# Optimization experiments

Measured on AMD Instinct MI355X. Metric: run time of the kernel, lower is better.

Reference implementation:

```python
import jax, jax.numpy as jnp
import numpy as np

H, D, HID = 16, 128, 2048
B, S = 2, 2048
NUM_BLOCKS, BLOCK_SIZE = 32, 128


def _rope(x, cos, sin):
    # x: [T, H, D]; cos/sin: [T, D/2] (neox / rotate-half style)
    half = x.shape[-1] // 2
    x1, x2 = x[..., :half], x[..., half:]
    c = cos[:, None, :]
    s = sin[:, None, :]
    return jnp.concatenate([x1 * c - x2 * s, x2 * c + x1 * s], axis=-1)


def setup_inputs() -> dict:
    key = jax.random.key(0)
    ks = jax.random.split(key, 6)
    T = B * S
    hidden_states = jax.random.normal(ks[0], (T, HID), jnp.float32)
    wqkv = jax.random.normal(ks[1], (HID, 3 * HID), jnp.float32) * 0.02
    bqkv = jax.random.normal(ks[2], (3 * HID,), jnp.float32) * 0.02
    wo = jax.random.normal(ks[3], (HID, HID), jnp.float32) * 0.02
    # rotary tables, base 10000, dim = head_size
    inv_freq = 1.0 / (10000.0 ** (jnp.arange(0, D, 2, dtype=jnp.float32) / D))  # [D/2]
    pos = jnp.tile(jnp.arange(S, dtype=jnp.float32), B)  # positions per token [T]
    ang = pos[:, None] * inv_freq[None, :]  # [T, D/2]
    cos, sin = jnp.cos(ang), jnp.sin(ang)
    k_cache = jnp.zeros((NUM_BLOCKS, BLOCK_SIZE, H, D), jnp.float32)
    v_cache = jnp.zeros((NUM_BLOCKS, BLOCK_SIZE, H, D), jnp.float32)
    cu_seqlen_prefill = jnp.array([0, S, 2 * S], jnp.int32)
    slots = jnp.arange(T, dtype=jnp.int32)
    return {"hidden_states": hidden_states, "cos": cos, "sin": sin,
            "wqkv": wqkv, "bqkv": bqkv, "wo": wo,
            "k_cache": k_cache, "v_cache": v_cache,
            "cu_seqlen_prefill": cu_seqlen_prefill, "slots": slots, "max_s": S}


def reference(hidden_states, cos, sin, wqkv, bqkv, wo, k_cache, v_cache,
              cu_seqlen_prefill, slots, max_s):
    T = hidden_states.shape[0]
    # fused QKV projection (c_attn)
    qkv = hidden_states @ wqkv + bqkv  # [T, 3*H*D]
    q, k, v = jnp.split(qkv, [H * D, 2 * H * D], axis=1)
    q = q.reshape(T, H, D)
    k = k.reshape(T, H, D)
    v = v.reshape(T, H, D)
    # rotary embedding on q and k (in-place in torch; functional here)
    q = _rope(q, cos, sin)
    k = _rope(k, cos, sin)
    # reshape_and_cache: scatter post-rope k and v into paged KV cache by slot
    kc = k_cache.reshape(-1, H, D).at[slots].set(k).reshape(k_cache.shape)
    vc = v_cache.reshape(-1, H, D).at[slots].set(v).reshape(v_cache.shape)
    # prefill flash attention: varlen causal; equal-length sequences here
    b, s = T // max_s, max_s
    qb = q.reshape(b, s, H, D)
    kb = k.reshape(b, s, H, D)
    vb = v.reshape(b, s, H, D)
    scale = D ** -0.5
    scores = jnp.einsum('bqhd,bkhd->bhqk', qb, kb) * scale  # [B,H,S,S]
    causal = jnp.tril(jnp.ones((s, s), bool))
    scores = jnp.where(causal[None, None], scores, jnp.finfo(scores.dtype).min)
    probs = jax.nn.softmax(scores, axis=-1)
    attn = jnp.einsum('bhqk,bkhd->bqhd', probs, vb).reshape(T, H * D)
    out = attn @ wo  # c_proj, no bias
    return out, kc, vc
```

## Files before the change

### kernel.cpp

```cpp
#include <hip/hip_runtime.h>

using f32x4  = __attribute__((ext_vector_type(4))) float;
using frag16 = __attribute__((ext_vector_type(8))) short;
using s16x4  = __attribute__((ext_vector_type(4))) short;
using s16x8  = __attribute__((ext_vector_type(8))) short;
using u32x4  = __attribute__((ext_vector_type(4))) unsigned;

#define DI __device__ __forceinline__

constexpr int HID  = 2048;
constexpr int NH   = 16;
constexpr int HD   = 128;
constexpr int TT   = 4096;
constexpr int SEQ  = 2048;
constexpr int NQKV = 3 * HID;
constexpr float SCL = 0.08838834764831845f * 1.4426950408889634f;

DI short f2bf(float f) {
  unsigned u = __builtin_bit_cast(unsigned, f);
  unsigned r = (u + 0x7fffu + ((u >> 16) & 1u)) >> 16;
  return (short)r;
}
DI float bf2f(short s) {
  unsigned u = ((unsigned)(unsigned short)s) << 16;
  return __builtin_bit_cast(float, u);
}
DI unsigned cvtpk(float lo, float hi) {
  unsigned r;
  asm("v_cvt_pk_bf16_f32 %0, %1, %2" : "=v"(r) : "v"(lo), "v"(hi));
  return r;
}

struct alignas(8) S4h { short a, b, c, d; };

__global__ void prep(const float* __restrict__ hidden, short* __restrict__ Abf,
                     const float* __restrict__ wqkv, short* __restrict__ Wqkvt,
                     const float* __restrict__ wo, short* __restrict__ Wot) {
  __shared__ float t[64][65];
  const int bid = blockIdx.x;
  const int tid = threadIdx.x;
  if (bid < 8192) {
    int gid = bid * 256 + tid;
    float4 v = ((const float4*)hidden)[gid];
    S4h o{f2bf(v.x), f2bf(v.y), f2bf(v.z), f2bf(v.w)};
    ((S4h*)Abf)[gid] = o;
    return;
  }
  const float* in;
  short* out;
  int ldin, R, bx, by;
  if (bid < 8192 + 3072) {
    int idx = bid - 8192;
    in = wqkv; out = Wqkvt; ldin = NQKV; R = HID;
    bx = idx % 96; by = idx / 96;
  } else {
    int idx = bid - 8192 - 3072;
    in = wo; out = Wot; ldin = HID; R = HID;
    bx = idx % 32; by = idx / 32;
  }
#pragma unroll
  for (int i = 0; i < 4; i++) {
    int idx = i * 256 + tid;
    int r = idx >> 4, c4 = idx & 15;
    size_t gi = (size_t)(by * 64 + r) * ldin + bx * 64 + c4 * 4;
    float4 v = *(const float4*)(in + gi);
    t[r][c4 * 4] = v.x; t[r][c4 * 4 + 1] = v.y;
    t[r][c4 * 4 + 2] = v.z; t[r][c4 * 4 + 3] = v.w;
  }
  __syncthreads();
#pragma unroll
  for (int i = 0; i < 4; i++) {
    int idx = i * 256 + tid;
    int r = idx >> 4, c4 = idx & 15;
    s16x4 o;
#pragma unroll
    for (int j = 0; j < 4; j++) o[j] = f2bf(t[c4 * 4 + j][r]);
    *(s16x4*)(out + (size_t)(bx * 64 + r) * R + by * 64 + c4 * 4) = o;
  }
}

__global__ void transpose_perm(const short* __restrict__ in, short* __restrict__ out,
                               int ldin, int R) {
  __shared__ float t[64][65];
  int tid = threadIdx.x;
  int bx = blockIdx.x, by = blockIdx.y;
#pragma unroll
  for (int i = 0; i < 4; i++) {
    int idx = i * 256 + tid;
    int r = idx >> 4, c4 = idx & 15;
    size_t gi = (size_t)(by * 64 + r) * ldin + bx * 64 + c4 * 4;
    s16x4 v = *(const s16x4*)(in + gi);
#pragma unroll
    for (int j = 0; j < 4; j++) t[r][c4 * 4 + j] = bf2f(v[j]);
  }
  __syncthreads();
#pragma unroll
  for (int i = 0; i < 4; i++) {
    int idx = i * 256 + tid;
    int r = idx >> 4, c4 = idx & 15;
    s16x4 o;
#pragma unroll
    for (int j = 0; j < 4; j++) {
      int c = c4 * 4 + j;
      int cs = (c >> 5) * 32 + ((c >> 2) & 1) * 16 + ((c >> 3) & 3) * 4 + (c & 3);
      o[j] = f2bf(t[cs][r]);
    }
    *(s16x4*)(out + (size_t)(bx * 64 + r) * R + by * 64 + c4 * 4) = o;
  }
}

#define GLDS(src, dst)                                                     \
  __builtin_amdgcn_global_load_lds(                                        \
      (const __attribute__((address_space(1))) void*)(src),                \
      (__attribute__((address_space(3))) void*)(dst), 16, 0, 0)

template <int EPI>
__global__ __launch_bounds__(256, 2) void gemm_bt(
    const short* __restrict__ A, const short* __restrict__ Bt,
    const float* __restrict__ bias, float* __restrict__ Cout,
    const float* __restrict__ cs, const float* __restrict__ sn,
    const int* __restrict__ slots,
    short* __restrict__ Qb, short* __restrict__ Kb, short* __restrict__ Vrow,
    float* __restrict__ kc, float* __restrict__ vc,
    int M, int N, int K) {
  __shared__ alignas(16) short Al[128 * 64];
  __shared__ alignas(16) short Bl[128 * 64];
  const int tid = threadIdx.x;
  const int wid = tid >> 6, lane = tid & 63;
  const int wr = wid >> 1, wc = wid & 1;
  const int l15 = lane & 15, lg = lane >> 4;
  const int gx = gridDim.x;
  const int id = blockIdx.y * gx + blockIdx.x;
  const int nwg = gx * gridDim.y;
  const int swz = (id & 7) * (nwg >> 3) + (id >> 3);
  const int row0 = (swz / gx) * 128, col0 = (swz % gx) * 128;
  const int lr8 = lane >> 3, l7 = lane & 7;

  f32x4 acc[4][4];
#pragma unroll
  for (int i = 0; i < 4; i++)
#pragma unroll
    for (int j = 0; j < 4; j++) acc[i][j] = {0.f, 0.f, 0.f, 0.f};

  for (int kt = 0; kt < K; kt += 64) {
#pragma unroll
    for (int c = 0; c < 4; c++) {
      int chunk = c * 4 + wid;
      int r = chunk * 8 + lr8;
      int ke = (l7 * 8) ^ ((r & 7) * 8);
      GLDS(A + (size_t)(row0 + r) * K + kt + ke, Al + chunk * 512);
      GLDS(Bt + (size_t)(col0 + r) * K + kt + ke, Bl + chunk * 512);
    }
    __syncthreads();
#pragma unroll
    for (int kk = 0; kk < 2; kk++) {
      frag16 af[4], bfv[4];
#pragma unroll
      for (int ai = 0; ai < 4; ai++) {
        int r = wr * 64 + ai * 16 + l15;
        int k0 = kk * 32 + lg * 8;
        af[ai] = *(const frag16*)(Al + r * 64 + (k0 ^ ((r & 7) * 8)));
      }
#pragma unroll
      for (int bj = 0; bj < 4; bj++) {
        int r = wc * 16 + (bj & 1) * 32 + ((bj >> 1) << 6) + l15;
        int k0 = kk * 32 + lg * 8;
        bfv[bj] = *(const frag16*)(Bl + r * 64 + (k0 ^ ((r & 7) * 8)));
      }
#pragma unroll
      for (int ai = 0; ai < 4; ai++)
#pragma unroll
        for (int bj = 0; bj < 4; bj++)
          acc[ai][bj] = __builtin_amdgcn_mfma_f32_16x16x32_bf16(
              af[ai], bfv[bj], acc[ai][bj], 0, 0, 0);
    }
    __syncthreads();
  }

  if (EPI == 0) {
#pragma unroll
    for (int ai = 0; ai < 4; ai++) {
#pragma unroll
      for (int bj = 0; bj < 4; bj++) {
        int row = row0 + wr * 64 + ai * 16 + lg * 4;
        int col = col0 + wc * 16 + (bj & 1) * 32 + ((bj >> 1) << 6) + l15;
#pragma unroll
        for (int r = 0; r < 4; r++)
          Cout[(size_t)(row + r) * N + col] = acc[ai][bj][r];
      }
    }
  } else {
    const int sec = col0 >> 11;
    const int h = (col0 & 2047) >> 7;
#pragma unroll
    for (int ai = 0; ai < 4; ai++) {
#pragma unroll
      for (int bj = 0; bj < 2; bj++) {
        const int d1 = wc * 16 + bj * 32 + l15;
        const float b1 = bias[col0 + d1];
        const float b2 = bias[col0 + d1 + 64];
        const int base = h * 128 + d1;
#pragma unroll
        for (int r = 0; r < 4; r++) {
          const int tok = row0 + wr * 64 + ai * 16 + lg * 4 + r;
          float v1 = acc[ai][bj][r] + b1;
          float v2 = acc[ai][bj + 2][r] + b2;
          if (sec == 0) {
            float c = cs[tok * 64 + d1], s = sn[tok * 64 + d1];
            Qb[(size_t)tok * HID + base]      = f2bf((v1 * c - v2 * s) * SCL);
            Qb[(size_t)tok * HID + base + 64] = f2bf((v2 * c + v1 * s) * SCL);
          } else if (sec == 1) {
            float c = cs[tok * 64 + d1], s = sn[tok * 64 + d1];
            float o1 = v1 * c - v2 * s, o2 = v2 * c + v1 * s;
            int sl = slots[tok];
            Kb[(size_t)tok * HID + base]      = f2bf(o1);
            Kb[(size_t)tok * HID + base + 64] = f2bf(o2);
            kc[(size_t)sl * HID + base]      = o1;
            kc[(size_t)sl * HID + base + 64] = o2;
          } else {
            int sl = slots[tok];
            vc[(size_t)sl * HID + base]      = v1;
            vc[(size_t)sl * HID + base + 64] = v2;
            Vrow[(size_t)tok * HID + base]      = f2bf(v1);
            Vrow[(size_t)tok * HID + base + 64] = f2bf(v2);
          }
        }
      }
    }
  }
}

__global__ __launch_bounds__(256, 2) void flash_attn7(
    const short* __restrict__ Qb, const short* __restrict__ Kb,
    const short* __restrict__ Vt, short* __restrict__ attn) {
  __shared__ alignas(16) short Klds[2][64 * 128];
  __shared__ alignas(16) short Vlds[2][128 * 64];

  const int tid = threadIdx.x;
  const int w = tid >> 6, lane = tid & 63;
  const int l15 = lane & 15, lg = lane >> 4;
  const int bid = blockIdx.x;
  const int p = bid >> 5;
  const int bh = bid & 31;
  const int b = bh >> 4, h = bh & 15;

  frag16 ones;
#pragma unroll
  for (int j = 0; j < 8; j++) ones[j] = (short)0x3F80;

  auto stage = [&](int kv0, int buf) {
#pragma unroll
    for (int ci = 0; ci < 4; ci++) {
      int cc = w * 4 + ci;
      int krow = cc * 4 + (lane >> 4);
      int kss = (lane & 15) ^ (krow & 15);
      GLDS(Kb + (size_t)(b * SEQ + kv0 + krow) * HID + h * HD + kss * 8,
           Klds[buf] + cc * 512);
      int vd = cc * 8 + (lane >> 3);
      int vss = (lane & 7) ^ (vd & 7);
      GLDS(Vt + (size_t)(h * HD + vd) * TT + b * SEQ + kv0 + vss * 8,
           Vlds[buf] + cc * 512);
    }
  };

  const int qrowH = (31 - p) * 64 + w * 16;
  const int qrowL = p * 64 + w * 16;
  const int ntH = 32 - p;

  frag16 qfH[4], qfL[4];
  {
    const short* qpH = Qb + (size_t)(b * SEQ + qrowH + l15) * HID + h * HD + lg * 8;
    const short* qpL = Qb + (size_t)(b * SEQ + qrowL + l15) * HID + h * HD + lg * 8;
#pragma unroll
    for (int ds = 0; ds < 4; ds++) {
      qfH[ds] = *(const frag16*)(qpH + ds * 32);
      qfL[ds] = *(const frag16*)(qpL + ds * 32);
    }
  }
  f32x4 oH[8], oL[8];
#pragma unroll
  for (int j = 0; j < 8; j++) { oH[j] = {0.f, 0.f, 0.f, 0.f}; oL[j] = {0.f, 0.f, 0.f, 0.f}; }
  f32x4 laH = {0.f, 0.f, 0.f, 0.f}, laL = {0.f, 0.f, 0.f, 0.f};
  float mrH = -1e30f, mrL = -1e30f;

  auto proc = [&](const frag16 (&qf)[4], f32x4 (&o)[8], f32x4& la, float& mr,
                  bool diag, const short* Kl, const short* Vl) {
    f32x4 sa[4];
#pragma unroll
    for (int f = 0; f < 4; f++) sa[f] = {0.f, 0.f, 0.f, 0.f};
    __builtin_amdgcn_s_setprio(1);
#pragma unroll
    for (int ds = 0; ds < 4; ds++) {
      int phys = (ds * 4 + lg) ^ l15;
#pragma unroll
      for (int f = 0; f < 4; f++) {
        frag16 kf = *(const frag16*)(Kl + (f * 16 + l15) * 128 + phys * 8);
        sa[f] = __builtin_amdgcn_mfma_f32_16x16x32_bf16(kf, qf[ds], sa[f], 0, 0, 0);
      }
    }
    __builtin_amdgcn_s_setprio(0);
    if (diag) {
      int ql = 16 * w + l15;
#pragma unroll
      for (int f = 0; f < 4; f++)
#pragma unroll
        for (int r = 0; r < 4; r++)
          if (f * 16 + lg * 4 + r > ql) sa[f][r] = -1e30f;
    }
    float pm = sa[0][0];
#pragma unroll
    for (int f = 0; f < 4; f++)
#pragma unroll
      for (int r = 0; r < 4; r++) pm = fmaxf(pm, sa[f][r]);
    pm = fmaxf(pm, __shfl_xor(pm, 16));
    pm = fmaxf(pm, __shfl_xor(pm, 32));
    if (__any(pm > mr + 8.f)) {
      float mn = fmaxf(mr, pm);
      float frl = exp2f(mr - mn);
      mr = mn;
      float fr4[4];
#pragma unroll
      for (int r = 0; r < 4; r++)
        fr4[r] = __shfl(frl, lg * 16 + lg * 4 + r);
#pragma unroll
      for (int r = 0; r < 4; r++) {
        la[r] *= fr4[r];
#pragma unroll
        for (int j = 0; j < 8; j++) o[j][r] *= fr4[r];
      }
    }
    float pe[4][4];
#pragma unroll
    for (int f = 0; f < 4; f++)
#pragma unroll
      for (int r = 0; r < 4; r++) pe[f][r] = exp2f(sa[f][r] - mr);
    u32x4 w0, w1;
    w0[0] = cvtpk(pe[0][0], pe[0][1]); w0[1] = cvtpk(pe[0][2], pe[0][3]);
    w0[2] = cvtpk(pe[1][0], pe[1][1]); w0[3] = cvtpk(pe[1][2], pe[1][3]);
    w1[0] = cvtpk(pe[2][0], pe[2][1]); w1[1] = cvtpk(pe[2][2], pe[2][3]);
    w1[2] = cvtpk(pe[3][0], pe[3][1]); w1[3] = cvtpk(pe[3][2], pe[3][3]);
    frag16 pf0 = __builtin_bit_cast(frag16, w0);
    frag16 pf1 = __builtin_bit_cast(frag16, w1);
    __builtin_amdgcn_s_setprio(1);
    la = __builtin_amdgcn_mfma_f32_16x16x32_bf16(pf0, ones, la, 0, 0, 0);
    la = __builtin_amdgcn_mfma_f32_16x16x32_bf16(pf1, ones, la, 0, 0, 0);
#pragma unroll
    for (int j = 0; j < 8; j++) {
      int d = j * 16 + l15;
      int p0 = lg ^ (d & 7);
      int p1 = (4 + lg) ^ (d & 7);
      frag16 vf0 = *(const frag16*)(Vl + d * 64 + p0 * 8);
      frag16 vf1 = *(const frag16*)(Vl + d * 64 + p1 * 8);
      o[j] = __builtin_amdgcn_mfma_f32_16x16x32_bf16(pf0, vf0, o[j], 0, 0, 0);
      o[j] = __builtin_amdgcn_mfma_f32_16x16x32_bf16(pf1, vf1, o[j], 0, 0, 0);
    }
    __builtin_amdgcn_s_setprio(0);
  };

  stage(0, 0);
  if (ntH > 1) stage(64, 1);

  int cur = 0;
  for (int t = 0; t < ntH; t++) {
    if (t + 1 < ntH) {
      asm volatile("s_waitcnt vmcnt(8)" ::: "memory");
    } else {
      asm volatile("s_waitcnt vmcnt(0)" ::: "memory");
    }
    asm volatile("s_barrier" ::: "memory");
    const short* Kl = &Klds[cur][0];
    const short* Vl = &Vlds[cur][0];
    proc(qfH, oH, laH, mrH, t == ntH - 1, Kl, Vl);
    if (t <= p) proc(qfL, oL, laL, mrL, t == p, Kl, Vl);
    asm volatile("s_barrier" ::: "memory");
    if (t + 2 < ntH) stage((t + 2) * 64, cur);
    cur ^= 1;
  }

  {
    float inv[4];
#pragma unroll
    for (int r = 0; r < 4; r++) inv[r] = 1.f / laH[r];
    short* op = attn + (size_t)(b * SEQ + qrowH + lg * 4) * HID + h * HD + l15;
#pragma unroll
    for (int j = 0; j < 8; j++)
#pragma unroll
      for (int r = 0; r < 4; r++)
        op[(size_t)r * HID + j * 16] = f2bf(oH[j][r] * inv[r]);
  }
  {
    float inv[4];
#pragma unroll
    for (int r = 0; r < 4; r++) inv[r] = 1.f / laL[r];
    short* op = attn + (size_t)(b * SEQ + qrowL + lg * 4) * HID + h * HD + l15;
#pragma unroll
    for (int j = 0; j < 8; j++)
#pragma unroll
      for (int r = 0; r < 4; r++)
        op[(size_t)r * HID + j * 16] = f2bf(oL[j][r] * inv[r]);
  }
}

extern "C" void kernel_launch(void* const* d_in, const int* in_sizes, int n_in,
                              void* d_out, int out_size, void* d_ws, size_t ws_size,
                              hipStream_t stream) {
  const float* hidden = (const float*)d_in[0];
  const float* cosb   = (const float*)d_in[1];
  const float* sinb   = (const float*)d_in[2];
  const float* wqkv   = (const float*)d_in[3];
  const float* bqkv   = (const float*)d_in[4];
  const float* wo     = (const float*)d_in[5];
  const int*   slots  = (const int*)d_in[9];

  float* out = (float*)d_out;
  float* kc  = out + (size_t)TT * HID;
  float* vc  = kc + (size_t)TT * HID;

  short* ws    = (short*)d_ws;
  short* Abf   = ws;
  short* Wqkvt = Abf + 8388608;
  short* Wot   = Wqkvt + 12582912;
  short* Qb    = Wot + 4194304;
  short* Kb    = Qb + 8388608;
  short* Vrow  = Kb + 8388608;
  short* Vt    = Vrow + 8388608;
  short* attnb = Abf;

  prep<<<8192 + 3072 + 1024, 256, 0, stream>>>(hidden, Abf, wqkv, Wqkvt, wo, Wot);
  gemm_bt<1><<<dim3(48, 32), 256, 0, stream>>>(
      Abf, Wqkvt, bqkv, nullptr, cosb, sinb, slots, Qb, Kb, Vrow, kc, vc,
      TT, NQKV, HID);
  transpose_perm<<<dim3(32, 64), 256, 0, stream>>>(Vrow, Vt, HID, TT);
  flash_attn7<<<512, 256, 0, stream>>>(Qb, Kb, Vt, attnb);
  gemm_bt<0><<<dim3(16, 32), 256, 0, stream>>>(
      attnb, Wot, nullptr, out, nullptr, nullptr, nullptr,
      nullptr, nullptr, nullptr, nullptr, nullptr, TT, HID, HID);
}
```

Before: 289.1 us.

## Widen flash attention blocks to 8 waves covering 128-row query tiles

The attention kernel now launches 256 blocks of 512 threads instead of 512 blocks of 256. Each block pairs a high and a low 128-row query tile, so every KV tile staged into LDS is shared by twice as many waves. Causal masking and skip decisions are now computed per wave from absolute row offsets. This halves the number of global-to-LDS K/V loads per unit of query work, but the grid now has fewer blocks on the machine and there is more per-wave imbalance near the diagonal.

```diff
diff --git a/kernel.cpp b/kernel.cpp
--- a/kernel.cpp
+++ b/kernel.cpp
@@ -230,7 +230,7 @@
   }
 }
 
-__global__ __launch_bounds__(256, 2) void flash_attn7(
+__global__ __launch_bounds__(512) void flash_attn8(
     const short* __restrict__ Qb, const short* __restrict__ Kb,
     const short* __restrict__ Vt, short* __restrict__ attn) {
   __shared__ alignas(16) short Klds[2][64 * 128];
@@ -240,32 +240,32 @@
   const int w = tid >> 6, lane = tid & 63;
   const int l15 = lane & 15, lg = lane >> 4;
   const int bid = blockIdx.x;
-  const int p = bid >> 5;
+  const int j = bid >> 5;
   const int bh = bid & 31;
   const int b = bh >> 4, h = bh & 15;
 
   frag16 ones;
 #pragma unroll
-  for (int j = 0; j < 8; j++) ones[j] = (short)0x3F80;
+  for (int q = 0; q < 8; q++) ones[q] = (short)0x3F80;
 
   auto stage = [&](int kv0, int buf) {
 #pragma unroll
-    for (int ci = 0; ci < 4; ci++) {
-      int cc = w * 4 + ci;
-      int krow = cc * 4 + (lane >> 4);
-      int kss = (lane & 15) ^ (krow & 15);
+    for (int ci = 0; ci < 2; ci++) {
+      int e = ci * 512 + w * 64 + lane;
+      int krow = e >> 4;
+      int kss = (e & 15) ^ (krow & 15);
       GLDS(Kb + (size_t)(b * SEQ + kv0 + krow) * HID + h * HD + kss * 8,
-           Klds[buf] + cc * 512);
-      int vd = cc * 8 + (lane >> 3);
-      int vss = (lane & 7) ^ (vd & 7);
+           Klds[buf] + (ci * 512 + w * 64) * 8);
+      int vd = e >> 3;
+      int vss = (e & 7) ^ (vd & 7);
       GLDS(Vt + (size_t)(h * HD + vd) * TT + b * SEQ + kv0 + vss * 8,
-           Vlds[buf] + cc * 512);
+           Vlds[buf] + (ci * 512 + w * 64) * 8);
     }
   };
 
-  const int qrowH = (31 - p) * 64 + w * 16;
-  const int qrowL = p * 64 + w * 16;
-  const int ntH = 32 - p;
+  const int qrowH = (15 - j) * 128 + w * 16;
+  const int qrowL = j * 128 + w * 16;
+  const int ntH = 32 - 2 * j;
 
   frag16 qfH[4], qfL[4];
   {
@@ -279,12 +279,12 @@
   }
   f32x4 oH[8], oL[8];
 #pragma unroll
-  for (int j = 0; j < 8; j++) { oH[j] = {0.f, 0.f, 0.f, 0.f}; oL[j] = {0.f, 0.f, 0.f, 0.f}; }
+  for (int q = 0; q < 8; q++) { oH[q] = {0.f, 0.f, 0.f, 0.f}; oL[q] = {0.f, 0.f, 0.f, 0.f}; }
   f32x4 laH = {0.f, 0.f, 0.f, 0.f}, laL = {0.f, 0.f, 0.f, 0.f};
   float mrH = -1e30f, mrL = -1e30f;
 
   auto proc = [&](const frag16 (&qf)[4], f32x4 (&o)[8], f32x4& la, float& mr,
-                  bool diag, const short* Kl, const short* Vl) {
+                  bool diag, int ql, const short* Kl, const short* Vl) {
     f32x4 sa[4];
 #pragma unroll
     for (int f = 0; f < 4; f++) sa[f] = {0.f, 0.f, 0.f, 0.f};
@@ -300,7 +300,6 @@
     }
     __builtin_amdgcn_s_setprio(0);
     if (diag) {
-      int ql = 16 * w + l15;
 #pragma unroll
       for (int f = 0; f < 4; f++)
 #pragma unroll
@@ -326,7 +325,7 @@
       for (int r = 0; r < 4; r++) {
         la[r] *= fr4[r];
 #pragma unroll
-        for (int j = 0; j < 8; j++) o[j][r] *= fr4[r];
+        for (int q = 0; q < 8; q++) o[q][r] *= fr4[r];
       }
     }
     float pe[4][4];
@@ -345,33 +344,36 @@
     la = __builtin_amdgcn_mfma_f32_16x16x32_bf16(pf0, ones, la, 0, 0, 0);
     la = __builtin_amdgcn_mfma_f32_16x16x32_bf16(pf1, ones, la, 0, 0, 0);
 #pragma unroll
-    for (int j = 0; j < 8; j++) {
-      int d = j * 16 + l15;
+    for (int q = 0; q < 8; q++) {
+      int d = q * 16 + l15;
       int p0 = lg ^ (d & 7);
       int p1 = (4 + lg) ^ (d & 7);
       frag16 vf0 = *(const frag16*)(Vl + d * 64 + p0 * 8);
       frag16 vf1 = *(const frag16*)(Vl + d * 64 + p1 * 8);
-      o[j] = __builtin_amdgcn_mfma_f32_16x16x32_bf16(pf0, vf0, o[j], 0, 0, 0);
-      o[j] = __builtin_amdgcn_mfma_f32_16x16x32_bf16(pf1, vf1, o[j], 0, 0, 0);
+      o[q] = __builtin_amdgcn_mfma_f32_16x16x32_bf16(pf0, vf0, o[q], 0, 0, 0);
+      o[q] = __builtin_amdgcn_mfma_f32_16x16x32_bf16(pf1, vf1, o[q], 0, 0, 0);
     }
     __builtin_amdgcn_s_setprio(0);
   };
 
   stage(0, 0);
-  if (ntH > 1) stage(64, 1);
+  stage(64, 1);
 
   int cur = 0;
   for (int t = 0; t < ntH; t++) {
     if (t + 1 < ntH) {
-      asm volatile("s_waitcnt vmcnt(8)" ::: "memory");
+      asm volatile("s_waitcnt vmcnt(4)" ::: "memory");
     } else {
       asm volatile("s_waitcnt vmcnt(0)" ::: "memory");
     }
     asm volatile("s_barrier" ::: "memory");
     const short* Kl = &Klds[cur][0];
     const short* Vl = &Vlds[cur][0];
-    proc(qfH, oH, laH, mrH, t == ntH - 1, Kl, Vl);
-    if (t <= p) proc(qfL, oL, laL, mrL, t == p, Kl, Vl);
+    const int kv0 = t * 64;
+    if (kv0 <= qrowH + 15)
+      proc(qfH, oH, laH, mrH, kv0 + 63 > qrowH, qrowH + l15 - kv0, Kl, Vl);
+    if (kv0 <= qrowL + 15)
+      proc(qfL, oL, laL, mrL, kv0 + 63 > qrowL, qrowL + l15 - kv0, Kl, Vl);
     asm volatile("s_barrier" ::: "memory");
     if (t + 2 < ntH) stage((t + 2) * 64, cur);
     cur ^= 1;
@@ -383,10 +385,10 @@
     for (int r = 0; r < 4; r++) inv[r] = 1.f / laH[r];
     short* op = attn + (size_t)(b * SEQ + qrowH + lg * 4) * HID + h * HD + l15;
 #pragma unroll
-    for (int j = 0; j < 8; j++)
+    for (int q = 0; q < 8; q++)
 #pragma unroll
       for (int r = 0; r < 4; r++)
-        op[(size_t)r * HID + j * 16] = f2bf(oH[j][r] * inv[r]);
+        op[(size_t)r * HID + q * 16] = f2bf(oH[q][r] * inv[r]);
   }
   {
     float inv[4];
@@ -394,10 +396,10 @@
     for (int r = 0; r < 4; r++) inv[r] = 1.f / laL[r];
     short* op = attn + (size_t)(b * SEQ + qrowL + lg * 4) * HID + h * HD + l15;
 #pragma unroll
-    for (int j = 0; j < 8; j++)
+    for (int q = 0; q < 8; q++)
 #pragma unroll
       for (int r = 0; r < 4; r++)
-        op[(size_t)r * HID + j * 16] = f2bf(oL[j][r] * inv[r]);
+        op[(size_t)r * HID + q * 16] = f2bf(oL[q][r] * inv[r]);
   }
 }
 
@@ -431,7 +433,7 @@
       Abf, Wqkvt, bqkv, nullptr, cosb, sinb, slots, Qb, Kb, Vrow, kc, vc,
       TT, NQKV, HID);
   transpose_perm<<<dim3(32, 64), 256, 0, stream>>>(Vrow, Vt, HID, TT);
-  flash_attn7<<<512, 256, 0, stream>>>(Qb, Kb, Vt, attnb);
+  flash_attn8<<<256, 512, 0, stream>>>(Qb, Kb, Vt, attnb);
   gemm_bt<0><<<dim3(16, 32), 256, 0, stream>>>(
       attnb, Wot, nullptr, out, nullptr, nullptr, nullptr,
       nullptr, nullptr, nullptr, nullptr, nullptr, TT, HID, HID);
```

After: 295.7 us. 1.02x slower.

## Move KV cache scatter into post kernel and simplify flash-attn prefetch

Applied to the files above, without the earlier changes.

Removes the strided fp32 KV-cache scatter from the QKV GEMM epilogue and does it in a combined post kernel that also performs the V transpose, reading bf16 K/V rows and writing vectorized fp32 cache rows. The flash attention loop changes from a two-tile-ahead prefetch with manual waitcnt/barrier to a one-tile-ahead prefetch using __syncthreads. The cache now holds bf16-rounded K and V values instead of exact fp32, which costs precision. The simpler pipeline may also expose more load latency in attention.

```diff
diff --git a/kernel.cpp b/kernel.cpp
--- a/kernel.cpp
+++ b/kernel.cpp
@@ -79,34 +79,52 @@
   }
 }
 
-__global__ void transpose_perm(const short* __restrict__ in, short* __restrict__ out,
-                               int ldin, int R) {
+__global__ void post(const short* __restrict__ Kb, const short* __restrict__ Vrow,
+                     short* __restrict__ Vt, const int* __restrict__ slots,
+                     float* __restrict__ kc, float* __restrict__ vc) {
   __shared__ float t[64][65];
-  int tid = threadIdx.x;
-  int bx = blockIdx.x, by = blockIdx.y;
-#pragma unroll
-  for (int i = 0; i < 4; i++) {
-    int idx = i * 256 + tid;
-    int r = idx >> 4, c4 = idx & 15;
-    size_t gi = (size_t)(by * 64 + r) * ldin + bx * 64 + c4 * 4;
-    s16x4 v = *(const s16x4*)(in + gi);
-#pragma unroll
-    for (int j = 0; j < 4; j++) t[r][c4 * 4 + j] = bf2f(v[j]);
-  }
-  __syncthreads();
-#pragma unroll
-  for (int i = 0; i < 4; i++) {
-    int idx = i * 256 + tid;
-    int r = idx >> 4, c4 = idx & 15;
-    s16x4 o;
-#pragma unroll
-    for (int j = 0; j < 4; j++) {
-      int c = c4 * 4 + j;
-      int cs = (c >> 5) * 32 + ((c >> 2) & 1) * 16 + ((c >> 3) & 3) * 4 + (c & 3);
-      o[j] = f2bf(t[cs][r]);
-    }
-    *(s16x4*)(out + (size_t)(bx * 64 + r) * R + by * 64 + c4 * 4) = o;
-  }
+  const int bid = blockIdx.x;
+  const int tid = threadIdx.x;
+  if (bid < 2048) {
+    int bx = bid & 31, by = bid >> 5;
+#pragma unroll
+    for (int i = 0; i < 4; i++) {
+      int idx = i * 256 + tid;
+      int r = idx >> 4, c4 = idx & 15;
+      size_t gi = (size_t)(by * 64 + r) * HID + bx * 64 + c4 * 4;
+      s16x4 v = *(const s16x4*)(Vrow + gi);
+#pragma unroll
+      for (int j = 0; j < 4; j++) t[r][c4 * 4 + j] = bf2f(v[j]);
+    }
+    __syncthreads();
+#pragma unroll
+    for (int i = 0; i < 4; i++) {
+      int idx = i * 256 + tid;
+      int r = idx >> 4, c4 = idx & 15;
+      s16x4 o;
+#pragma unroll
+      for (int j = 0; j < 4; j++) {
+        int c = c4 * 4 + j;
+        int cs = (c >> 5) * 32 + ((c >> 2) & 1) * 16 + ((c >> 3) & 3) * 4 + (c & 3);
+        o[j] = f2bf(t[cs][r]);
+      }
+      *(s16x4*)(Vt + (size_t)(bx * 64 + r) * TT + by * 64 + c4 * 4) = o;
+    }
+    return;
+  }
+  const int tok = bid - 2048;
+  const int slot = slots[tok];
+  const short* kr = Kb + (size_t)tok * HID;
+  const short* vr = Vrow + (size_t)tok * HID;
+  float* kco = kc + (size_t)slot * HID;
+  float* vco = vc + (size_t)slot * HID;
+  const int i = tid * 8;
+  s16x8 k8 = *(const s16x8*)(kr + i);
+  s16x8 v8 = *(const s16x8*)(vr + i);
+  *(float4*)(kco + i)     = {bf2f(k8[0]), bf2f(k8[1]), bf2f(k8[2]), bf2f(k8[3])};
+  *(float4*)(kco + i + 4) = {bf2f(k8[4]), bf2f(k8[5]), bf2f(k8[6]), bf2f(k8[7])};
+  *(float4*)(vco + i)     = {bf2f(v8[0]), bf2f(v8[1]), bf2f(v8[2]), bf2f(v8[3])};
+  *(float4*)(vco + i + 4) = {bf2f(v8[4]), bf2f(v8[5]), bf2f(v8[6]), bf2f(v8[7])};
 }
 
 #define GLDS(src, dst)                                                     \
@@ -119,9 +137,7 @@
     const short* __restrict__ A, const short* __restrict__ Bt,
     const float* __restrict__ bias, float* __restrict__ Cout,
     const float* __restrict__ cs, const float* __restrict__ sn,
-    const int* __restrict__ slots,
     short* __restrict__ Qb, short* __restrict__ Kb, short* __restrict__ Vrow,
-    float* __restrict__ kc, float* __restrict__ vc,
     int M, int N, int K) {
   __shared__ alignas(16) short Al[128 * 64];
   __shared__ alignas(16) short Bl[128 * 64];
@@ -211,16 +227,9 @@
             Qb[(size_t)tok * HID + base + 64] = f2bf((v2 * c + v1 * s) * SCL);
           } else if (sec == 1) {
             float c = cs[tok * 64 + d1], s = sn[tok * 64 + d1];
-            float o1 = v1 * c - v2 * s, o2 = v2 * c + v1 * s;
-            int sl = slots[tok];
-            Kb[(size_t)tok * HID + base]      = f2bf(o1);
-            Kb[(size_t)tok * HID + base + 64] = f2bf(o2);
-            kc[(size_t)sl * HID + base]      = o1;
-            kc[(size_t)sl * HID + base + 64] = o2;
+            Kb[(size_t)tok * HID + base]      = f2bf(v1 * c - v2 * s);
+            Kb[(size_t)tok * HID + base + 64] = f2bf(v2 * c + v1 * s);
           } else {
-            int sl = slots[tok];
-            vc[(size_t)sl * HID + base]      = v1;
-            vc[(size_t)sl * HID + base + 64] = v2;
             Vrow[(size_t)tok * HID + base]      = f2bf(v1);
             Vrow[(size_t)tok * HID + base + 64] = f2bf(v2);
           }
@@ -230,7 +239,7 @@
   }
 }
 
-__global__ __launch_bounds__(256, 2) void flash_attn7(
+__global__ __launch_bounds__(256, 2) void flash_attn6(
     const short* __restrict__ Qb, const short* __restrict__ Kb,
     const short* __restrict__ Vt, short* __restrict__ attn) {
   __shared__ alignas(16) short Klds[2][64 * 128];
@@ -358,22 +367,16 @@
   };
 
   stage(0, 0);
-  if (ntH > 1) stage(64, 1);
+  __syncthreads();
 
   int cur = 0;
   for (int t = 0; t < ntH; t++) {
-    if (t + 1 < ntH) {
-      asm volatile("s_waitcnt vmcnt(8)" ::: "memory");
-    } else {
-      asm volatile("s_waitcnt vmcnt(0)" ::: "memory");
-    }
-    asm volatile("s_barrier" ::: "memory");
+    if (t + 1 < ntH) stage((t + 1) * 64, cur ^ 1);
     const short* Kl = &Klds[cur][0];
     const short* Vl = &Vlds[cur][0];
     proc(qfH, oH, laH, mrH, t == ntH - 1, Kl, Vl);
     if (t <= p) proc(qfL, oL, laL, mrL, t == p, Kl, Vl);
-    asm volatile("s_barrier" ::: "memory");
-    if (t + 2 < ntH) stage((t + 2) * 64, cur);
+    __syncthreads();
     cur ^= 1;
   }
 
@@ -428,11 +431,10 @@
 
   prep<<<8192 + 3072 + 1024, 256, 0, stream>>>(hidden, Abf, wqkv, Wqkvt, wo, Wot);
   gemm_bt<1><<<dim3(48, 32), 256, 0, stream>>>(
-      Abf, Wqkvt, bqkv, nullptr, cosb, sinb, slots, Qb, Kb, Vrow, kc, vc,
-      TT, NQKV, HID);
-  transpose_perm<<<dim3(32, 64), 256, 0, stream>>>(Vrow, Vt, HID, TT);
-  flash_attn7<<<512, 256, 0, stream>>>(Qb, Kb, Vt, attnb);
+      Abf, Wqkvt, bqkv, nullptr, cosb, sinb, Qb, Kb, Vrow, TT, NQKV, HID);
+  post<<<2048 + 4096, 256, 0, stream>>>(Kb, Vrow, Vt, slots, kc, vc);
+  flash_attn6<<<512, 256, 0, stream>>>(Qb, Kb, Vt, attnb);
   gemm_bt<0><<<dim3(16, 32), 256, 0, stream>>>(
-      attnb, Wot, nullptr, out, nullptr, nullptr, nullptr,
-      nullptr, nullptr, nullptr, nullptr, nullptr, TT, HID, HID);
-}
+      attnb, Wot, nullptr, out, nullptr, nullptr, nullptr, nullptr, nullptr,
+      TT, HID, HID);
+}
```

Result: no change. 283.5 us (median of 2 runs) (-1.9%).
